# Performance work log

Hardware: AMD Instinct MI355X
Metric: run time of the kernel (lower is better)

Reference implementation:

```python
import jax, jax.numpy as jnp
import numpy as np

B, T, D, H = 4, 2048, 1024, 16
DK = D // H

def setup_inputs() -> dict:
    key = jax.random.key(0)
    ks = jax.random.split(key, 9)
    s = 0.02
    return {
        "x": jax.random.normal(ks[0], (B, T, D), dtype=jnp.float32),
        "Wq": jax.random.normal(ks[1], (D, D), dtype=jnp.float32) * s,
        "bq": jnp.zeros((D,), dtype=jnp.float32),
        "Wk": jax.random.normal(ks[2], (D, D), dtype=jnp.float32) * s,
        "bk": jnp.zeros((D,), dtype=jnp.float32),
        "Wv": jax.random.normal(ks[3], (D, D), dtype=jnp.float32) * s,
        "bv": jnp.zeros((D,), dtype=jnp.float32),
        "Wo": jax.random.normal(ks[4], (D, D), dtype=jnp.float32) * s,
        "bo": jnp.zeros((D,), dtype=jnp.float32),
    }

def reference(x, Wq, bq, Wk, bk, Wv, bv, Wo, bo):
    b, t, c = x.shape
    # projections -> [B, H, T, DK]
    def split_heads(y):
        return y.reshape(b, t, H, DK).transpose(0, 2, 1, 3)
    q = split_heads(x @ Wq.T + bq)
    k = split_heads(x @ Wk.T + bk)
    v = split_heads(x @ Wv.T + bv)
    scale = 1.0 / jnp.sqrt(jnp.asarray(DK, dtype=x.dtype))
    scores = jnp.einsum("bhqd,bhkd->bhqk", q, k) * scale  # [B,H,T,T]
    causal = jnp.tril(jnp.ones((t, t), dtype=bool))
    scores = jnp.where(causal, scores, jnp.asarray(-jnp.inf, dtype=scores.dtype))
    attn = jax.nn.softmax(scores, axis=-1)
    out = jnp.einsum("bhqk,bhkd->bhqd", attn, v)  # [B,H,T,DK]
    out = out.transpose(0, 2, 1, 3).reshape(b, t, c)
    return out @ Wo.T + bo
```

## Files before the change

### kernel.cpp

```cpp
#include <hip/hip_runtime.h>
#include <hip/hip_bf16.h>

#define DEV __device__ __forceinline__

typedef unsigned short u16;
typedef unsigned int u32;
typedef __attribute__((ext_vector_type(4))) float f32x4;
typedef __attribute__((ext_vector_type(16))) float f32x16;
typedef __attribute__((ext_vector_type(8))) __bf16 bf16x8;
typedef __attribute__((ext_vector_type(8))) u16 u16x8;
typedef __attribute__((ext_vector_type(4))) u16 u16x4;
typedef __attribute__((ext_vector_type(4))) u32 u32x4;

#define CSCALE 0.18033688011112042f

DEV u16 f2bf(float f) {
    u32 u = __builtin_bit_cast(u32, f);
    u32 r = (u + 0x7fffu + ((u >> 16) & 1u)) >> 16;
    return (u16)r;
}

DEV u16 f2bf_fast(float f) {
    u32 u = __builtin_bit_cast(u32, f);
    return (u16)((u + 0x8000u) >> 16);
}

DEV float fastrcp(float x) {
#if __has_builtin(__builtin_amdgcn_rcpf)
    return __builtin_amdgcn_rcpf(x);
#else
    return 1.0f / x;
#endif
}

DEV u32 cvtpk_bf16(float lo, float hi) {
    u32 r;
    asm("v_cvt_pk_bf16_f32 %0, %1, %2" : "=v"(r) : "v"(lo), "v"(hi));
    return r;
}

DEV void plswap(u32& a, u32& b) {
    asm volatile("v_permlane32_swap_b32 %0, %1" : "+v"(a), "+v"(b));
}

DEV void gload_lds16(const void* g, void* l) {
    void* gg = const_cast<void*>(g);
    __builtin_amdgcn_global_load_lds(
        (const __attribute__((address_space(1))) void*)gg,
        (__attribute__((address_space(3))) void*)l,
        16, 0, 0);
}

DEV f32x16 mfma32(bf16x8 a, bf16x8 b, f32x16 c) {
    return __builtin_amdgcn_mfma_f32_32x32x16_bf16(a, b, c, 0, 0, 0);
}

__global__ void cvt_f32_bf16(const float* __restrict__ in, u16* __restrict__ out,
                             int n4, float scale) {
    int i = blockIdx.x * blockDim.x + threadIdx.x;
    if (i < n4) {
        float4 v = ((const float4*)in)[i];
        u16x4 o;
        o[0] = f2bf(v.x * scale); o[1] = f2bf(v.y * scale);
        o[2] = f2bf(v.z * scale); o[3] = f2bf(v.w * scale);
        ((u16x4*)out)[i] = o;
    }
}

__global__ void build_bias(const float* __restrict__ bq, const float* __restrict__ bk,
                           const float* __restrict__ bv, float* __restrict__ o) {
    int i = blockIdx.x * blockDim.x + threadIdx.x;
    if (i < 3072) {
        float v;
        if (i < 1024) v = bq[i] * CSCALE;
        else if (i < 2048) v = bk[i - 1024];
        else v = bv[i - 2048];
        o[i] = v;
    }
}

template<int F32OUT>
__global__ __launch_bounds__(256) void gemm_bt(
    const u16* __restrict__ A, const u16* __restrict__ B,
    const float* __restrict__ bias, void* __restrict__ Cv,
    int K, int ldc, int bnPerXcd)
{
    __shared__ u16 As[128 * 64];
    __shared__ u16 Bs[128 * 64];
    const int t = threadIdx.x;
    const int lane = t & 63;
    const int w = t >> 6;
    const int wm = w >> 1, wn = w & 1;
    const int id = (int)blockIdx.x;
    const int xcd = id & 7, r = id >> 3;
    const int bm = (r & 63) * 128;
    const int bn = (xcd * bnPerXcd + (r >> 6)) * 128;
    const int lr = lane & 15;
    const int lg = lane >> 4;

    f32x4 acc[4][4] = {};

    for (int k0 = 0; k0 < K; k0 += 64) {
        #pragma unroll
        for (int i = 0; i < 4; ++i) {
            int off = (t + i * 256) * 16;
            int row = off >> 7;
            int colb = off & 127;
            gload_lds16((const char*)A + ((size_t)(bm + row) * K + k0) * 2 + colb,
                        (char*)As + off);
            gload_lds16((const char*)B + ((size_t)(bn + row) * K + k0) * 2 + colb,
                        (char*)Bs + off);
        }
        __syncthreads();
        #pragma unroll
        for (int kk = 0; kk < 2; ++kk) {
            bf16x8 af[4], bfr[4];
            #pragma unroll
            for (int m = 0; m < 4; ++m)
                af[m] = *(const bf16x8*)&As[(wm * 64 + m * 16 + lr) * 64 + kk * 32 + lg * 8];
            #pragma unroll
            for (int n = 0; n < 4; ++n)
                bfr[n] = *(const bf16x8*)&Bs[(wn * 64 + n * 16 + lr) * 64 + kk * 32 + lg * 8];
            #pragma unroll
            for (int m = 0; m < 4; ++m)
                #pragma unroll
                for (int n = 0; n < 4; ++n)
                    acc[m][n] = __builtin_amdgcn_mfma_f32_16x16x32_bf16(af[m], bfr[n], acc[m][n], 0, 0, 0);
        }
        __syncthreads();
    }

    #pragma unroll
    for (int n = 0; n < 4; ++n) {
        int col = bn + wn * 64 + n * 16 + lr;
        float bv = bias[col];
        #pragma unroll
        for (int m = 0; m < 4; ++m) {
            int row0 = bm + wm * 64 + m * 16 + lg * 4;
            #pragma unroll
            for (int r2 = 0; r2 < 4; ++r2) {
                float v = acc[m][n][r2] + bv;
                size_t idx = (size_t)(row0 + r2) * ldc + col;
                if (F32OUT) ((float*)Cv)[idx] = v;
                else        ((u16*)Cv)[idx] = f2bf(v);
            }
        }
    }
}

__global__ __launch_bounds__(256, 2) void attn_fwd(
    const u16* __restrict__ QKV, u16* __restrict__ Om)
{
    constexpr int T = 2048, LD = 3072, DO = 1024;
    constexpr int PSTR = 72;
    constexpr float NEG = -3.0e38f;

    __shared__ __align__(16) u16 Ks[2][64 * 64];
    __shared__ __align__(16) u16 Vt[2][64 * PSTR];

    const int t = threadIdx.x, lane = t & 63, w = t >> 6;
    const int ql = lane & 31, hi = lane >> 5;

    const int id = (int)blockIdx.x;
    const int bh = (id & 7) * 8 + ((id >> 3) >> 3);
    const int xq = 7 - ((id >> 3) & 7);
    const int b = bh >> 4, h = bh & 15;
    const int q0s[2] = { (8 + xq) * 128, (7 - xq) * 128 };
    const size_t rowbase = (size_t)b * T * LD + h * 64;
    const u16* Qm = QKV + rowbase;
    const u16* Km = QKV + rowbase + 1024;
    const u16* Vm = QKV + rowbase + 2048;
    const int nt = q0s[0] / 64 + 2;

    int qg[2], qmax[2];
    #pragma unroll
    for (int ti = 0; ti < 2; ++ti) {
        qg[ti]   = q0s[ti] + w * 32 + ql;
        qmax[ti] = q0s[ti] + w * 32 + 31;
    }

    bf16x8 qf[2][4];
    #pragma unroll
    for (int ti = 0; ti < 2; ++ti) {
        const u16* qp = Qm + (size_t)qg[ti] * LD + hi * 8;
        #pragma unroll
        for (int s = 0; s < 4; ++s) qf[ti][s] = *(const bf16x8*)(qp + s * 16);
    }

    f32x16 oa[2][2] = {};
    float lsum[2] = { 0.f, 0.f };

    const int krow = t >> 3, kslot = t & 7;
    const u16* kCur = Km + (size_t)krow * LD + 8 * (kslot ^ (krow & 7));
    const int kv2 = (t & 31) * 2, dd = (t >> 5) * 8;
    const u16* vCur = Vm + (size_t)kv2 * LD + dd;
    u16x8 vva, vvb;

    auto stageK = [&](int buf) {
        u16* dst = (u16*)Ks + buf * 4096 + t * 8;
        gload_lds16(kCur, dst);
        gload_lds16(kCur + 32 * LD, dst + 2048);
        kCur += 64 * LD;
    };
    auto loadV = [&]() {
        vva = *(const u16x8*)vCur;
        vvb = *(const u16x8*)(vCur + LD);
        vCur += 64 * LD;
    };
    auto writeVt = [&](int buf) {
        u32* vd = (u32*)((u16*)Vt + buf * (64 * PSTR) + dd * PSTR + kv2);
        #pragma unroll
        for (int j = 0; j < 8; ++j)
            vd[j * (PSTR / 2)] = (u32)vva[j] | ((u32)vvb[j] << 16);
    };

    stageK(0);
    loadV();
    writeVt(0);

    for (int it0 = 0; it0 < nt; it0 += 2) {
        #pragma unroll
        for (int half = 0; half < 2; ++half) {
            const int BUF = half;
            const int it = it0 + half;
            const int kv0 = it * 64;
            __syncthreads();

            const bool more = (it + 1 < nt);
            if (more) { stageK(BUF ^ 1); loadV(); }

            const bool a0  = kv0 <= qmax[0],      a1  = kv0 <= qmax[1];
            const bool a0h = kv0 + 32 <= qmax[0], a1h = kv0 + 32 <= qmax[1];

            f32x16 sa[2][2] = {};
            __builtin_amdgcn_s_setprio(1);
            #pragma unroll
            for (int n = 0; n < 2; ++n) {
                const bool c0 = n ? a0h : a0;
                const bool c1 = n ? a1h : a1;
                if (!(c0 || c1)) continue;
                const int row = n * 32 + ql;
                const int swz = (row & 7) << 4;
                #pragma unroll
                for (int s = 0; s < 4; ++s) {
                    bf16x8 kf = *(const bf16x8*)((const char*)Ks + BUF * 8192 + row * 128 +
                                                 ((((s << 1) | hi) << 4) ^ swz));
                    if (c0) sa[0][n] = mfma32(kf, qf[0][s], sa[0][n]);
                    if (c1) sa[1][n] = mfma32(kf, qf[1][s], sa[1][n]);
                }
            }
            __builtin_amdgcn_s_setprio(0);

            u32x4 pw[2][2][2];
            #pragma unroll
            for (int ti = 0; ti < 2; ++ti) {
                if (kv0 > qmax[ti]) continue;
                const bool acth = (kv0 + 32 <= qmax[ti]);
                float rs = 0.f;
                #pragma unroll
                for (int n = 0; n < 2; ++n) {
                    if (n == 1 && !acth) continue;
                    if (kv0 + n * 32 + 31 + 4 * hi > q0s[ti] + w * 32) {
                        #pragma unroll
                        for (int r = 0; r < 16; ++r) {
                            int kvg = kv0 + n * 32 + (r & 3) + 8 * (r >> 2) + 4 * hi;
                            if (kvg > qg[ti]) sa[ti][n][r] = NEG;
                        }
                    }
                    float pv[16];
                    #pragma unroll
                    for (int r = 0; r < 16; ++r)
                        pv[r] = __builtin_exp2f(sa[ti][n][r]);
                    float s8[8];
                    #pragma unroll
                    for (int r = 0; r < 8; ++r) s8[r] = pv[r] + pv[r + 8];
                    rs += ((s8[0] + s8[4]) + (s8[1] + s8[5])) + ((s8[2] + s8[6]) + (s8[3] + s8[7]));
                    #pragma unroll
                    for (int s = 0; s < 2; ++s) {
                        u32 u0 = cvtpk_bf16(pv[8 * s + 0], pv[8 * s + 1]);
                        u32 u1 = cvtpk_bf16(pv[8 * s + 2], pv[8 * s + 3]);
                        u32 u2 = cvtpk_bf16(pv[8 * s + 4], pv[8 * s + 5]);
                        u32 u3 = cvtpk_bf16(pv[8 * s + 6], pv[8 * s + 7]);
                        plswap(u0, u2);
                        plswap(u1, u3);
                        pw[ti][n][s] = u32x4{u0, u1, u2, u3};
                    }
                }
                rs += __shfl_xor(rs, 32);
                lsum[ti] += rs;
            }

            __builtin_amdgcn_s_setprio(1);
            #pragma unroll
            for (int dt = 0; dt < 2; ++dt) {
                const int vrow = dt * 32 + ql;
                #pragma unroll
                for (int n = 0; n < 2; ++n) {
                    const bool c0 = n ? a0h : a0;
                    const bool c1 = n ? a1h : a1;
                    if (!(c0 || c1)) continue;
                    #pragma unroll
                    for (int s = 0; s < 2; ++s) {
                        bf16x8 vf = *(const bf16x8*)((const u16*)Vt + BUF * (64 * PSTR) +
                                                     vrow * PSTR + n * 32 + s * 16 + hi * 8);
                        if (c0) oa[0][dt] = mfma32(vf, __builtin_bit_cast(bf16x8, pw[0][n][s]), oa[0][dt]);
                        if (c1) oa[1][dt] = mfma32(vf, __builtin_bit_cast(bf16x8, pw[1][n][s]), oa[1][dt]);
                    }
                }
            }
            __builtin_amdgcn_s_setprio(0);

            if (more) writeVt(BUF ^ 1);
        }
    }

    __syncthreads();
    u16* ot = ((u16*)Vt) + w * (32 * PSTR);
    const int lq = lane >> 1, half2 = lane & 1;
    const size_t obase = (size_t)b * T * DO + h * 64;
    #pragma unroll
    for (int ti = 0; ti < 2; ++ti) {
        const float inv = fastrcp(lsum[ti]);
        #pragma unroll
        for (int dt = 0; dt < 2; ++dt)
            #pragma unroll
            for (int r = 0; r < 16; ++r) {
                int d = dt * 32 + (r & 3) + 8 * (r >> 2) + 4 * hi;
                ot[ql * PSTR + d] = f2bf_fast(oa[ti][dt][r] * inv);
            }
        const u16* src = ot + lq * PSTR + half2 * 32;
        u16* dst = Om + obase + (size_t)(q0s[ti] + w * 32 + lq) * DO + half2 * 32;
        #pragma unroll
        for (int seg = 0; seg < 4; ++seg)
            *(u16x8*)(dst + seg * 8) = *(const u16x8*)(src + seg * 8);
    }
}

extern "C" void kernel_launch(void* const* d_in, const int* in_sizes, int n_in,
                              void* d_out, int out_size, void* d_ws, size_t ws_size,
                              hipStream_t stream)
{
    const float* x  = (const float*)d_in[0];
    const float* Wq = (const float*)d_in[1];
    const float* bq = (const float*)d_in[2];
    const float* Wk = (const float*)d_in[3];
    const float* bk = (const float*)d_in[4];
    const float* Wv = (const float*)d_in[5];
    const float* bv = (const float*)d_in[6];
    const float* Wo = (const float*)d_in[7];
    const float* bo = (const float*)d_in[8];

    constexpr int T = 2048, D = 1024;
    constexpr size_t MT = (size_t)4 * T;

    const size_t NEED = (size_t)74 << 20;
    if (ws_size < NEED) return;

    char* ws = (char*)d_ws;
    u16* xb    = (u16*)(ws);
    u16* Ob    = (u16*)(ws);
    u16* Wqkvb = (u16*)(ws + ((size_t)16 << 20));
    u16* Wob   = (u16*)(ws + ((size_t)22 << 20));
    u16* QKVb  = (u16*)(ws + ((size_t)24 << 20));
    float* bqkv = (float*)(ws + ((size_t)72 << 20));

    int nx4 = (int)(MT * D / 4);
    cvt_f32_bf16<<<(nx4 + 255) / 256, 256, 0, stream>>>(x, xb, nx4, 1.0f);
    int nw4 = D * D / 4;
    cvt_f32_bf16<<<(nw4 + 255) / 256, 256, 0, stream>>>(Wq, Wqkvb, nw4, CSCALE);
    cvt_f32_bf16<<<(nw4 + 255) / 256, 256, 0, stream>>>(Wk, Wqkvb + (size_t)D * D, nw4, 1.0f);
    cvt_f32_bf16<<<(nw4 + 255) / 256, 256, 0, stream>>>(Wv, Wqkvb + (size_t)2 * D * D, nw4, 1.0f);
    cvt_f32_bf16<<<(nw4 + 255) / 256, 256, 0, stream>>>(Wo, Wob, nw4, 1.0f);
    build_bias<<<12, 256, 0, stream>>>(bq, bk, bv, bqkv);

    gemm_bt<0><<<dim3(1536), 256, 0, stream>>>(xb, Wqkvb, bqkv, QKVb, D, 3072, 3);

    attn_fwd<<<dim3(512), 256, 0, stream>>>(QKVb, Ob);

    gemm_bt<1><<<dim3(512), 256, 0, stream>>>(Ob, Wob, bo, d_out, D, 1024, 1);
}
```

Baseline: 216.6 us.

## Process one query tile per attention block and double the grid

The attention kernel no longer pairs two complementary causal query tiles per block to balance work. Each block now handles a single 128-row query tile, and blocks are ordered longest-first so the largest causal workloads are scheduled early. The grid doubles to 1024 blocks and launch bounds are raised to allow four blocks per CU, aiming for more occupancy and less register pressure. In exchange, each K/V tile loaded into shared memory is reused by half as many queries, and load balance now depends on scheduling order instead of pairing.

```diff
diff --git a/kernel.cpp b/kernel.cpp
--- a/kernel.cpp
+++ b/kernel.cpp
@@ -148,7 +148,7 @@
     }
 }
 
-__global__ __launch_bounds__(256, 2) void attn_fwd(
+__global__ __launch_bounds__(256, 4) void attn_fwd(
     const u16* __restrict__ QKV, u16* __restrict__ Om)
 {
     constexpr int T = 2048, LD = 3072, DO = 1024;
@@ -162,33 +162,28 @@
     const int ql = lane & 31, hi = lane >> 5;
 
     const int id = (int)blockIdx.x;
-    const int bh = (id & 7) * 8 + ((id >> 3) >> 3);
-    const int xq = 7 - ((id >> 3) & 7);
+    const int slot = id >> 6;
+    const int bh = (id & 7) * 8 + ((id >> 3) & 7);
+    const int q0 = (15 - slot) * 128;
     const int b = bh >> 4, h = bh & 15;
-    const int q0s[2] = { (8 + xq) * 128, (7 - xq) * 128 };
     const size_t rowbase = (size_t)b * T * LD + h * 64;
     const u16* Qm = QKV + rowbase;
     const u16* Km = QKV + rowbase + 1024;
     const u16* Vm = QKV + rowbase + 2048;
-    const int nt = q0s[0] / 64 + 2;
-
-    int qg[2], qmax[2];
-    #pragma unroll
-    for (int ti = 0; ti < 2; ++ti) {
-        qg[ti]   = q0s[ti] + w * 32 + ql;
-        qmax[ti] = q0s[ti] + w * 32 + 31;
-    }
-
-    bf16x8 qf[2][4];
-    #pragma unroll
-    for (int ti = 0; ti < 2; ++ti) {
-        const u16* qp = Qm + (size_t)qg[ti] * LD + hi * 8;
-        #pragma unroll
-        for (int s = 0; s < 4; ++s) qf[ti][s] = *(const bf16x8*)(qp + s * 16);
-    }
-
-    f32x16 oa[2][2] = {};
-    float lsum[2] = { 0.f, 0.f };
+    const int nt = q0 / 64 + 2;
+
+    const int qg = q0 + w * 32 + ql;
+    const int qmax = q0 + w * 32 + 31;
+
+    bf16x8 qf[4];
+    {
+        const u16* qp = Qm + (size_t)qg * LD + hi * 8;
+        #pragma unroll
+        for (int s = 0; s < 4; ++s) qf[s] = *(const bf16x8*)(qp + s * 16);
+    }
+
+    f32x16 oa[2] = {};
+    float lsum = 0.f;
 
     const int krow = t >> 3, kslot = t & 7;
     const u16* kCur = Km + (size_t)krow * LD + 8 * (kslot ^ (krow & 7));
@@ -229,48 +224,42 @@
             const bool more = (it + 1 < nt);
             if (more) { stageK(BUF ^ 1); loadV(); }
 
-            const bool a0  = kv0 <= qmax[0],      a1  = kv0 <= qmax[1];
-            const bool a0h = kv0 + 32 <= qmax[0], a1h = kv0 + 32 <= qmax[1];
-
-            f32x16 sa[2][2] = {};
+            const bool a0  = kv0 <= qmax;
+            const bool a0h = kv0 + 32 <= qmax;
+
+            f32x16 sa[2] = {};
             __builtin_amdgcn_s_setprio(1);
             #pragma unroll
             for (int n = 0; n < 2; ++n) {
-                const bool c0 = n ? a0h : a0;
-                const bool c1 = n ? a1h : a1;
-                if (!(c0 || c1)) continue;
+                if (!(n ? a0h : a0)) continue;
                 const int row = n * 32 + ql;
                 const int swz = (row & 7) << 4;
                 #pragma unroll
                 for (int s = 0; s < 4; ++s) {
                     bf16x8 kf = *(const bf16x8*)((const char*)Ks + BUF * 8192 + row * 128 +
                                                  ((((s << 1) | hi) << 4) ^ swz));
-                    if (c0) sa[0][n] = mfma32(kf, qf[0][s], sa[0][n]);
-                    if (c1) sa[1][n] = mfma32(kf, qf[1][s], sa[1][n]);
+                    sa[n] = mfma32(kf, qf[s], sa[n]);
                 }
             }
             __builtin_amdgcn_s_setprio(0);
 
-            u32x4 pw[2][2][2];
-            #pragma unroll
-            for (int ti = 0; ti < 2; ++ti) {
-                if (kv0 > qmax[ti]) continue;
-                const bool acth = (kv0 + 32 <= qmax[ti]);
+            u32x4 pw[2][2];
+            if (a0) {
                 float rs = 0.f;
                 #pragma unroll
                 for (int n = 0; n < 2; ++n) {
-                    if (n == 1 && !acth) continue;
-                    if (kv0 + n * 32 + 31 + 4 * hi > q0s[ti] + w * 32) {
+                    if (n == 1 && !a0h) continue;
+                    if (kv0 + n * 32 + 31 > q0 + w * 32) {
                         #pragma unroll
                         for (int r = 0; r < 16; ++r) {
                             int kvg = kv0 + n * 32 + (r & 3) + 8 * (r >> 2) + 4 * hi;
-                            if (kvg > qg[ti]) sa[ti][n][r] = NEG;
+                            if (kvg > qg) sa[n][r] = NEG;
                         }
                     }
                     float pv[16];
                     #pragma unroll
                     for (int r = 0; r < 16; ++r)
-                        pv[r] = __builtin_exp2f(sa[ti][n][r]);
+                        pv[r] = __builtin_exp2f(sa[n][r]);
                     float s8[8];
                     #pragma unroll
                     for (int r = 0; r < 8; ++r) s8[r] = pv[r] + pv[r + 8];
@@ -283,11 +272,11 @@
                         u32 u3 = cvtpk_bf16(pv[8 * s + 6], pv[8 * s + 7]);
                         plswap(u0, u2);
                         plswap(u1, u3);
-                        pw[ti][n][s] = u32x4{u0, u1, u2, u3};
+                        pw[n][s] = u32x4{u0, u1, u2, u3};
                     }
                 }
                 rs += __shfl_xor(rs, 32);
-                lsum[ti] += rs;
+                lsum += rs;
             }
 
             __builtin_amdgcn_s_setprio(1);
@@ -296,15 +285,12 @@
                 const int vrow = dt * 32 + ql;
                 #pragma unroll
                 for (int n = 0; n < 2; ++n) {
-                    const bool c0 = n ? a0h : a0;
-                    const bool c1 = n ? a1h : a1;
-                    if (!(c0 || c1)) continue;
+                    if (!(n ? a0h : a0)) continue;
                     #pragma unroll
                     for (int s = 0; s < 2; ++s) {
                         bf16x8 vf = *(const bf16x8*)((const u16*)Vt + BUF * (64 * PSTR) +
                                                      vrow * PSTR + n * 32 + s * 16 + hi * 8);
-                        if (c0) oa[0][dt] = mfma32(vf, __builtin_bit_cast(bf16x8, pw[0][n][s]), oa[0][dt]);
-                        if (c1) oa[1][dt] = mfma32(vf, __builtin_bit_cast(bf16x8, pw[1][n][s]), oa[1][dt]);
+                        oa[dt] = mfma32(vf, __builtin_bit_cast(bf16x8, pw[n][s]), oa[dt]);
                     }
                 }
             }
@@ -316,24 +302,21 @@
 
     __syncthreads();
     u16* ot = ((u16*)Vt) + w * (32 * PSTR);
-    const int lq = lane >> 1, half2 = lane & 1;
+    const float inv = fastrcp(lsum);
+    #pragma unroll
+    for (int dt = 0; dt < 2; ++dt)
+        #pragma unroll
+        for (int r = 0; r < 16; ++r) {
+            int d = dt * 32 + (r & 3) + 8 * (r >> 2) + 4 * hi;
+            ot[ql * PSTR + d] = f2bf_fast(oa[dt][r] * inv);
+        }
+    const int lq = lane >> 1, hv = lane & 1;
     const size_t obase = (size_t)b * T * DO + h * 64;
+    const u16* src = ot + lq * PSTR + hv * 32;
+    u16* dst = Om + obase + (size_t)(q0 + w * 32 + lq) * DO + hv * 32;
     #pragma unroll
-    for (int ti = 0; ti < 2; ++ti) {
-        const float inv = fastrcp(lsum[ti]);
-        #pragma unroll
-        for (int dt = 0; dt < 2; ++dt)
-            #pragma unroll
-            for (int r = 0; r < 16; ++r) {
-                int d = dt * 32 + (r & 3) + 8 * (r >> 2) + 4 * hi;
-                ot[ql * PSTR + d] = f2bf_fast(oa[ti][dt][r] * inv);
-            }
-        const u16* src = ot + lq * PSTR + half2 * 32;
-        u16* dst = Om + obase + (size_t)(q0s[ti] + w * 32 + lq) * DO + half2 * 32;
-        #pragma unroll
-        for (int seg = 0; seg < 4; ++seg)
-            *(u16x8*)(dst + seg * 8) = *(const u16x8*)(src + seg * 8);
-    }
+    for (int seg = 0; seg < 4; ++seg)
+        *(u16x8*)(dst + seg * 8) = *(const u16x8*)(src + seg * 8);
 }
 
 extern "C" void kernel_launch(void* const* d_in, const int* in_sizes, int n_in,
@@ -375,7 +358,7 @@
 
     gemm_bt<0><<<dim3(1536), 256, 0, stream>>>(xb, Wqkvb, bqkv, QKVb, D, 3072, 3);
 
-    attn_fwd<<<dim3(512), 256, 0, stream>>>(QKVb, Ob);
+    attn_fwd<<<dim3(1024), 256, 0, stream>>>(QKVb, Ob);
 
     gemm_bt<1><<<dim3(512), 256, 0, stream>>>(Ob, Wob, bo, d_out, D, 1024, 1);
 }
```

Measured after the change: 238.0 us. 9.9% more time.
